# Optimization experiments

Hardware: AMD Instinct MI355X
Metric: run time of the kernel (lower is better)

Reference implementation:

```python
import jax, jax.numpy as jnp
import numpy as np

B, S, N = 128, 64, 32          # batch, self nodes, neighbors per node
INP_CAPS, OUT_CAPS, CAP_SZ = 8, 8, 16
K = OUT_CAPS
D = OUT_CAPS * CAP_SZ          # 128
C = D // K                     # capsule dim = 16
TAU = 1.0
EPS = 1e-12                    # F.normalize eps


def _l2norm(x):
    n = jnp.sqrt(jnp.sum(x * x, axis=-1, keepdims=True))
    return x / jnp.maximum(n, EPS)


def setup_inputs() -> dict:
    key = jax.random.key(0)
    k1, k2, k3, k4 = jax.random.split(key, 4)
    inp_d = INP_CAPS * CAP_SZ
    return {
        "self_vectors": jax.random.normal(k1, (B, S, inp_d), dtype=jnp.float32),
        "neighbor_vectors": jax.random.normal(k2, (B, S, N, inp_d), dtype=jnp.float32),
        "w1": jax.random.normal(k3, (inp_d, D), dtype=jnp.float32) * (1.0 / np.sqrt(inp_d)),
        "b1": jax.random.normal(k4, (D,), dtype=jnp.float32) * (1.0 / np.sqrt(D)),
        "max_iter": 3,
    }


def reference(self_vectors, neighbor_vectors, w1, b1, max_iter):
    inp_d = INP_CAPS * CAP_SZ
    self_z = jax.nn.relu(self_vectors.reshape(-1, inp_d) @ w1 + b1)
    neigh_z = jax.nn.relu(neighbor_vectors.reshape(-1, inp_d) @ w1 + b1)

    # [B,S,K,C] and [B,S,N,K,C], each capsule L2-normalized
    self_zn = _l2norm(self_z.reshape(B, S, K, C))
    neigh_zn = _l2norm(neigh_z.reshape(B, S, N, K, C))

    u = None
    for it in range(max_iter):
        if u is None:
            p = jnp.zeros((B, S, N, K), dtype=self_zn.dtype)
        else:
            # agreement scores: [B,S,N,K]
            p = jnp.einsum("bsnkc,bskc->bsnk", neigh_zn, u)
        p = jax.nn.softmax(p / TAU, axis=-1)
        # weighted neighbor sum over N -> [B,S,K,C]
        u = jnp.einsum("bsnkc,bsnk->bskc", neigh_zn, p) + self_zn
        if it < max_iter - 1:
            u = _l2norm(u)

    # dropout p=0.0 (eval) -> identity
    return jax.nn.relu(u.reshape(B, S, D))
```

## Files before the change

### kernel.cpp

```cpp
#include <hip/hip_runtime.h>
#include <hip/hip_bf16.h>


#define NB 32
#define DD 128
#define ZS 132
#define PPS 37


#define WSYNC() asm volatile("s_waitcnt lgkmcnt(0)" ::: "memory")

typedef __attribute__((ext_vector_type(8))) short bf16x8;
typedef __attribute__((ext_vector_type(4))) float f32x4;
typedef __attribute__((ext_vector_type(4))) float float4v;

__device__ __forceinline__ float bf16bits_to_f32(unsigned short u) {
  return __uint_as_float(((unsigned int)u) << 16);
}
__device__ __forceinline__ void split_bf16(float x, unsigned short& hi, unsigned short& lo) {
  unsigned int xb = __float_as_uint(x);
  hi = (unsigned short)(xb >> 16);
  float hif = __uint_as_float(xb & 0xFFFF0000u);
  float lof = x - hif;
  lo = (unsigned short)(__float_as_uint(lof) >> 16);
}
__device__ __forceinline__ void make_frag(float4v v0, float4v v1, bf16x8& h, bf16x8& l) {
#pragma unroll
  for (int i = 0; i < 4; ++i) {
    unsigned short hh, ll;
    split_bf16(v0[i], hh, ll);
    h[i] = (short)hh; l[i] = (short)ll;
    split_bf16(v1[i], hh, ll);
    h[4 + i] = (short)hh; l[4 + i] = (short)ll;
  }
}

__global__ void detect_kernel(const unsigned short* __restrict__ w1u,
                              int* __restrict__ flag) {
  int t = threadIdx.x;
  float v = bf16bits_to_f32(w1u[2 * t]);
  int hit = !(fabsf(v) < 1e4f);
  unsigned long long m = __ballot(hit);
  if (t == 0) flag[0] = (m != 0ull) ? 1 : 0;
}

__global__ __launch_bounds__(256) void swizzle_w_kernel(
    const void* __restrict__ w1, const int* __restrict__ flag,
    unsigned short* __restrict__ whi, unsigned short* __restrict__ wlo) {
  int idx = blockIdx.x * 256 + threadIdx.x;
  int k = idx >> 7, n = idx & 127;
  int kt = k >> 5, q = (k >> 3) & 3, j = k & 7;
  int nt = n >> 4, nl = n & 15;
  int lane = q * 16 + nl;
  int dst = ((kt * 8 + nt) * 64 + lane) * 8 + j;
  unsigned short hb, lb;
  if (*flag) {
    split_bf16(((const float*)w1)[idx], hb, lb);
  } else {
    hb = ((const unsigned short*)w1)[idx];
    lb = 0;
  }
  whi[dst] = hb;
  wlo[dst] = lb;
}

__global__ __launch_bounds__(64, 2) void routing_kernel(
    const void* __restrict__ selfv,
    const void* __restrict__ neighv,
    const unsigned short* __restrict__ whi,
    const unsigned short* __restrict__ wlo,
    const void* __restrict__ b1,
    void* __restrict__ out,
    const int* __restrict__ flag) {
  __shared__ __align__(16) float zn[33 * ZS];
  __shared__ __align__(16) float nrm[264];
  __shared__ __align__(16) float pp[8 * PPS];
  __shared__ __align__(16) float uu[128];

  const int lane = threadIdx.x;
  const int q = lane >> 4;
  const int ml = lane & 15;
  const size_t bs = blockIdx.x;
  const bool isf32 = (*flag != 0);

  const size_t noff = bs * (size_t)(NB * DD);
  const size_t soff = bs * (size_t)DD;

  f32x4 acc[3][8];
#pragma unroll
  for (int mt = 0; mt < 3; ++mt)
#pragma unroll
    for (int nt = 0; nt < 8; ++nt) acc[mt][nt] = (f32x4){0.f, 0.f, 0.f, 0.f};

#pragma unroll
  for (int kt = 0; kt < 4; ++kt) {
    const int col = kt * 32 + q * 8;
    bf16x8 a0h, a0l, a1h, a1l, a2h, a2l;
    if (isf32) {
      const float* nf = (const float*)neighv + noff;
      const float* sf = (const float*)selfv + soff;
      float4v v0 = *(const float4v*)(nf + (size_t)ml * DD + col);
      float4v v1 = *(const float4v*)(nf + (size_t)ml * DD + col + 4);
      make_frag(v0, v1, a0h, a0l);
      v0 = *(const float4v*)(nf + (size_t)(16 + ml) * DD + col);
      v1 = *(const float4v*)(nf + (size_t)(16 + ml) * DD + col + 4);
      make_frag(v0, v1, a1h, a1l);
      v0 = *(const float4v*)(sf + col);
      v1 = *(const float4v*)(sf + col + 4);
      make_frag(v0, v1, a2h, a2l);
    } else {
      const unsigned short* nbf = (const unsigned short*)neighv + noff;
      const unsigned short* sbf = (const unsigned short*)selfv + soff;
      const bf16x8 zv = (bf16x8){0, 0, 0, 0, 0, 0, 0, 0};
      a0h = *(const bf16x8*)(nbf + (size_t)ml * DD + col);
      a1h = *(const bf16x8*)(nbf + (size_t)(16 + ml) * DD + col);
      a2h = *(const bf16x8*)(sbf + col);
      a0l = zv; a1l = zv; a2l = zv;
    }
#pragma unroll
    for (int nt = 0; nt < 8; ++nt) {
      const size_t bo = ((size_t)(kt * 8 + nt) * 64 + lane) * 8;
      bf16x8 bh = *(const bf16x8*)(whi + bo);
      bf16x8 bl = *(const bf16x8*)(wlo + bo);
      acc[0][nt] = __builtin_amdgcn_mfma_f32_16x16x32_bf16(a0h, bh, acc[0][nt], 0, 0, 0);
      acc[1][nt] = __builtin_amdgcn_mfma_f32_16x16x32_bf16(a1h, bh, acc[1][nt], 0, 0, 0);
      acc[2][nt] = __builtin_amdgcn_mfma_f32_16x16x32_bf16(a2h, bh, acc[2][nt], 0, 0, 0);
      acc[0][nt] = __builtin_amdgcn_mfma_f32_16x16x32_bf16(a0h, bl, acc[0][nt], 0, 0, 0);
      acc[1][nt] = __builtin_amdgcn_mfma_f32_16x16x32_bf16(a1h, bl, acc[1][nt], 0, 0, 0);
      acc[2][nt] = __builtin_amdgcn_mfma_f32_16x16x32_bf16(a2h, bl, acc[2][nt], 0, 0, 0);
      acc[0][nt] = __builtin_amdgcn_mfma_f32_16x16x32_bf16(a0l, bh, acc[0][nt], 0, 0, 0);
      acc[1][nt] = __builtin_amdgcn_mfma_f32_16x16x32_bf16(a1l, bh, acc[1][nt], 0, 0, 0);
      acc[2][nt] = __builtin_amdgcn_mfma_f32_16x16x32_bf16(a2l, bh, acc[2][nt], 0, 0, 0);
    }
  }

  float bias[8];
#pragma unroll
  for (int nt = 0; nt < 8; ++nt) {
    const int c = nt * 16 + ml;
    bias[nt] = isf32 ? ((const float*)b1)[c]
                     : bf16bits_to_f32(((const unsigned short*)b1)[c]);
  }
#pragma unroll
  for (int mt = 0; mt < 2; ++mt)
#pragma unroll
    for (int nt = 0; nt < 8; ++nt)
#pragma unroll
      for (int r = 0; r < 4; ++r) {
        const int row = mt * 16 + q * 4 + r;
        zn[row * ZS + nt * 16 + ml] = fmaxf(acc[mt][nt][r] + bias[nt], 0.f);
      }
  if (q == 0) {
#pragma unroll
    for (int nt = 0; nt < 8; ++nt)
      zn[32 * ZS + nt * 16 + ml] = fmaxf(acc[2][nt][0] + bias[nt], 0.f);
  }
  WSYNC();

  for (int id = lane; id < 264; id += 64) {
    const int row = id >> 3, k = id & 7;
    const float4v* zp = (const float4v*)&zn[row * ZS + k * 16];
    float4v a = zp[0], b = zp[1], c = zp[2], d = zp[3];
    float ss = a[0]*a[0]+a[1]*a[1]+a[2]*a[2]+a[3]*a[3]
             + b[0]*b[0]+b[1]*b[1]+b[2]*b[2]+b[3]*b[3]
             + c[0]*c[0]+c[1]*c[1]+c[2]*c[2]+c[3]*c[3]
             + d[0]*d[0]+d[1]*d[1]+d[2]*d[2]+d[3]*d[3];
    nrm[id] = 1.f / fmaxf(sqrtf(ss), 1e-12f);
  }
  WSYNC();

  const int half = lane >> 5;
  const int k2 = (lane >> 2) & 7;
  const int c4 = lane & 3;
  const int k1 = lane & 7;
  const int ng = lane >> 3;

  for (int it = 0; it < 3; ++it) {
    if (it > 0) {
      const float4v* up = (const float4v*)&uu[k1 * 16];
      float4v U0 = up[0], U1 = up[1], U2 = up[2], U3 = up[3];
#pragma unroll
      for (int p = 0; p < 4; ++p) {
        const int n = ng + 8 * p;
        const float4v* zp = (const float4v*)&zn[n * ZS + k1 * 16];
        float4v z0 = zp[0], z1 = zp[1], z2 = zp[2], z3 = zp[3];
        float dot = U0[0]*z0[0]+U0[1]*z0[1]+U0[2]*z0[2]+U0[3]*z0[3]
                  + U1[0]*z1[0]+U1[1]*z1[1]+U1[2]*z1[2]+U1[3]*z1[3]
                  + U2[0]*z2[0]+U2[1]*z2[1]+U2[2]*z2[2]+U2[3]*z2[3]
                  + U3[0]*z3[0]+U3[1]*z3[1]+U3[2]*z3[2]+U3[3]*z3[3];
        const float nv = nrm[n * 8 + k1];
        const float lg = dot * nv;
        float m = lg;
        m = fmaxf(m, __shfl_xor(m, 1));
        m = fmaxf(m, __shfl_xor(m, 2));
        m = fmaxf(m, __shfl_xor(m, 4));
        float e = __expf(lg - m);
        float s = e;
        s += __shfl_xor(s, 1);
        s += __shfl_xor(s, 2);
        s += __shfl_xor(s, 4);
        pp[k1 * PPS + n] = (e / s) * nv;
      }
      WSYNC();
    }
    float4v a = (float4v){0.f, 0.f, 0.f, 0.f};
#pragma unroll
    for (int n0 = 0; n0 < 16; ++n0) {
      const int n = half * 16 + n0;
      const float w = (it == 0) ? nrm[n * 8 + k2] * 0.125f : pp[k2 * PPS + n];
      float4v z = *(const float4v*)&zn[n * ZS + k2 * 16 + c4 * 4];
      a[0] += w * z[0];
      a[1] += w * z[1];
      a[2] += w * z[2];
      a[3] += w * z[3];
    }
#pragma unroll
    for (int i = 0; i < 4; ++i) a[i] += __shfl_xor(a[i], 32);
    {
      float4v zs = *(const float4v*)&zn[32 * ZS + k2 * 16 + c4 * 4];
      const float sn = nrm[256 + k2];
      a[0] += sn * zs[0];
      a[1] += sn * zs[1];
      a[2] += sn * zs[2];
      a[3] += sn * zs[3];
    }
    if (it < 2) {
      float ss = a[0]*a[0] + a[1]*a[1] + a[2]*a[2] + a[3]*a[3];
      ss += __shfl_xor(ss, 1);
      ss += __shfl_xor(ss, 2);
      const float rn = 1.f / fmaxf(sqrtf(ss), 1e-12f);
      a[0] *= rn; a[1] *= rn; a[2] *= rn; a[3] *= rn;
      if (half == 0) *(float4v*)&uu[k2 * 16 + c4 * 4] = a;
      WSYNC();
    } else if (half == 0) {
      a[0] = (a[0] < 0.f) ? 0.f : a[0];
      a[1] = (a[1] < 0.f) ? 0.f : a[1];
      a[2] = (a[2] < 0.f) ? 0.f : a[2];
      a[3] = (a[3] < 0.f) ? 0.f : a[3];
      const size_t oidx = bs * DD + k2 * 16 + c4 * 4;
      if (isf32) {
        *(float4v*)((float*)out + oidx) = a;
      } else {
        unsigned int w0, w1;
        unsigned int x0 = __float_as_uint(a[0]);
        unsigned int x1 = __float_as_uint(a[1]);
        unsigned int x2 = __float_as_uint(a[2]);
        unsigned int x3 = __float_as_uint(a[3]);
        x0 += 0x7fffu + ((x0 >> 16) & 1u);
        x1 += 0x7fffu + ((x1 >> 16) & 1u);
        x2 += 0x7fffu + ((x2 >> 16) & 1u);
        x3 += 0x7fffu + ((x3 >> 16) & 1u);
        w0 = (x0 >> 16) | (x1 & 0xFFFF0000u);
        w1 = (x2 >> 16) | (x3 & 0xFFFF0000u);
        ((unsigned int*)out)[oidx / 2] = w0;
        ((unsigned int*)out)[oidx / 2 + 1] = w1;
      }
    }
  }
}

extern "C" void kernel_launch(void* const* d_in, const int* in_sizes, int n_in,
                              void* d_out, int out_size, void* d_ws, size_t ws_size,
                              hipStream_t stream) {
  (void)in_sizes; (void)n_in; (void)out_size; (void)ws_size;
  const void* selfv = d_in[0];
  const void* neighv = d_in[1];
  const void* w1 = d_in[2];
  const void* b1 = d_in[3];
  int* flag = (int*)d_ws;
  unsigned short* whi = (unsigned short*)((char*)d_ws + 64);
  unsigned short* wlo = (unsigned short*)((char*)d_ws + 64 + 32768);

  detect_kernel<<<1, 64, 0, stream>>>((const unsigned short*)w1, flag);
  swizzle_w_kernel<<<64, 256, 0, stream>>>(w1, flag, whi, wlo);
  routing_kernel<<<8192, 64, 0, stream>>>(selfv, neighv, whi, wlo, b1, d_out, flag);
}
```

Baseline: 242.5 us.

## Split self-capsule GEMM into separate kernel and keep routing in MFMA registers

Self-vector projection and normalization move into a new batched kernel that writes normalized self capsules to the output buffer. The routing kernel then computes only the 32 neighbor rows and runs all routing iterations directly on the MFMA accumulator registers, using DPP 16-lane reductions instead of LDS staging. This removes shared memory and the wasted third MFMA tile, so more blocks can be resident per CU. In exchange it adds an extra kernel launch plus a global round-trip for the self capsules, and the softmax weights are rounded to bf16 with the max-subtraction dropped.

```diff
diff --git a/kernel.cpp b/kernel.cpp
--- a/kernel.cpp
+++ b/kernel.cpp
@@ -2,13 +2,7 @@
 #include <hip/hip_bf16.h>
 
 
-#define NB 32
 #define DD 128
-#define ZS 132
-#define PPS 37
-
-
-#define WSYNC() asm volatile("s_waitcnt lgkmcnt(0)" ::: "memory")
 
 typedef __attribute__((ext_vector_type(8))) short bf16x8;
 typedef __attribute__((ext_vector_type(4))) float f32x4;
@@ -33,6 +27,29 @@
     split_bf16(v1[i], hh, ll);
     h[4 + i] = (short)hh; l[4 + i] = (short)ll;
   }
+}
+
+template <int CTRL>
+__device__ __forceinline__ float dpp_add(float x) {
+  int y = __builtin_amdgcn_update_dpp(0, __float_as_int(x), CTRL, 0xf, 0xf, true);
+  return x + __int_as_float(y);
+}
+__device__ __forceinline__ float sum16(float x) {
+  x = dpp_add<0xB1>(x);
+  x = dpp_add<0x4E>(x);
+  x = dpp_add<0x124>(x);
+  x = dpp_add<0x128>(x);
+  return x;
+}
+
+__device__ __forceinline__ unsigned pack_bf16(float a, float b) {
+  return (__float_as_uint(a) >> 16) | (__float_as_uint(b) & 0xFFFF0000u);
+}
+__device__ __forceinline__ float unpack_lo(unsigned w) {
+  return __uint_as_float(w << 16);
+}
+__device__ __forceinline__ float unpack_hi(unsigned w) {
+  return __uint_as_float(w & 0xFFFF0000u);
 }
 
 __global__ void detect_kernel(const unsigned short* __restrict__ w1u,
@@ -64,58 +81,115 @@
   wlo[dst] = lb;
 }
 
-__global__ __launch_bounds__(64, 2) void routing_kernel(
+__global__ __launch_bounds__(64, 4) void selfz_kernel(
     const void* __restrict__ selfv,
+    const unsigned short* __restrict__ whi,
+    const unsigned short* __restrict__ wlo,
+    const void* __restrict__ b1,
+    void* __restrict__ out,
+    const int* __restrict__ flag) {
+  const int lane = threadIdx.x;
+  const int q = lane >> 4, ml = lane & 15;
+  const int base = blockIdx.x * 16;
+  const bool isf32 = (*flag != 0);
+
+  f32x4 acc[8];
+#pragma unroll
+  for (int nt = 0; nt < 8; ++nt) acc[nt] = (f32x4){0.f, 0.f, 0.f, 0.f};
+
+#pragma unroll
+  for (int kt = 0; kt < 4; ++kt) {
+    const int col = kt * 32 + q * 8;
+    bf16x8 ah, al;
+    if (isf32) {
+      const float* sf = (const float*)selfv + (size_t)(base + ml) * DD + col;
+      make_frag(*(const float4v*)sf, *(const float4v*)(sf + 4), ah, al);
+    } else {
+      ah = *(const bf16x8*)((const unsigned short*)selfv + (size_t)(base + ml) * DD + col);
+      al = (bf16x8){0, 0, 0, 0, 0, 0, 0, 0};
+    }
+#pragma unroll
+    for (int nt = 0; nt < 8; ++nt) {
+      const size_t bo = ((size_t)(kt * 8 + nt) * 64 + lane) * 8;
+      bf16x8 bh = *(const bf16x8*)(whi + bo);
+      bf16x8 bl = *(const bf16x8*)(wlo + bo);
+      acc[nt] = __builtin_amdgcn_mfma_f32_16x16x32_bf16(ah, bh, acc[nt], 0, 0, 0);
+      acc[nt] = __builtin_amdgcn_mfma_f32_16x16x32_bf16(ah, bl, acc[nt], 0, 0, 0);
+      acc[nt] = __builtin_amdgcn_mfma_f32_16x16x32_bf16(al, bh, acc[nt], 0, 0, 0);
+    }
+  }
+#pragma unroll
+  for (int nt = 0; nt < 8; ++nt) {
+    const float bv = isf32 ? ((const float*)b1)[nt * 16 + ml]
+                           : bf16bits_to_f32(((const unsigned short*)b1)[nt * 16 + ml]);
+#pragma unroll
+    for (int r = 0; r < 4; ++r) acc[nt][r] = fmaxf(acc[nt][r] + bv, 0.f);
+  }
+#pragma unroll
+  for (int r = 0; r < 4; ++r)
+#pragma unroll
+    for (int nt = 0; nt < 8; ++nt) {
+      float ss = sum16(acc[nt][r] * acc[nt][r]);
+      acc[nt][r] *= 1.f / fmaxf(sqrtf(ss), 1e-12f);
+    }
+#pragma unroll
+  for (int r = 0; r < 4; ++r)
+#pragma unroll
+    for (int nt = 0; nt < 8; ++nt) {
+      const size_t o = (size_t)(base + q * 4 + r) * DD + nt * 16 + ml;
+      if (isf32) {
+        ((float*)out)[o] = acc[nt][r];
+      } else {
+        unsigned int xb = __float_as_uint(acc[nt][r]);
+        ((unsigned short*)out)[o] =
+            (unsigned short)((xb + 0x7fffu + ((xb >> 16) & 1u)) >> 16);
+      }
+    }
+}
+
+__global__ __launch_bounds__(64, 4) void routing_kernel(
     const void* __restrict__ neighv,
     const unsigned short* __restrict__ whi,
     const unsigned short* __restrict__ wlo,
     const void* __restrict__ b1,
     void* __restrict__ out,
     const int* __restrict__ flag) {
-  __shared__ __align__(16) float zn[33 * ZS];
-  __shared__ __align__(16) float nrm[264];
-  __shared__ __align__(16) float pp[8 * PPS];
-  __shared__ __align__(16) float uu[128];
-
   const int lane = threadIdx.x;
-  const int q = lane >> 4;
-  const int ml = lane & 15;
+  const int q = lane >> 4, ml = lane & 15;
   const size_t bs = blockIdx.x;
   const bool isf32 = (*flag != 0);
 
-  const size_t noff = bs * (size_t)(NB * DD);
-  const size_t soff = bs * (size_t)DD;
-
-  f32x4 acc[3][8];
-#pragma unroll
-  for (int mt = 0; mt < 3; ++mt)
+  float zs[8];
+#pragma unroll
+  for (int nt = 0; nt < 8; ++nt) {
+    const size_t o = bs * DD + nt * 16 + ml;
+    zs[nt] = isf32 ? ((const float*)out)[o]
+                   : bf16bits_to_f32(((const unsigned short*)out)[o]);
+  }
+
+  f32x4 acc[2][8];
+#pragma unroll
+  for (int mt = 0; mt < 2; ++mt)
 #pragma unroll
     for (int nt = 0; nt < 8; ++nt) acc[mt][nt] = (f32x4){0.f, 0.f, 0.f, 0.f};
 
+  const size_t noff = bs * (size_t)(32 * DD);
 #pragma unroll
   for (int kt = 0; kt < 4; ++kt) {
     const int col = kt * 32 + q * 8;
-    bf16x8 a0h, a0l, a1h, a1l, a2h, a2l;
+    bf16x8 a0h, a0l, a1h, a1l;
     if (isf32) {
       const float* nf = (const float*)neighv + noff;
-      const float* sf = (const float*)selfv + soff;
-      float4v v0 = *(const float4v*)(nf + (size_t)ml * DD + col);
-      float4v v1 = *(const float4v*)(nf + (size_t)ml * DD + col + 4);
-      make_frag(v0, v1, a0h, a0l);
-      v0 = *(const float4v*)(nf + (size_t)(16 + ml) * DD + col);
-      v1 = *(const float4v*)(nf + (size_t)(16 + ml) * DD + col + 4);
-      make_frag(v0, v1, a1h, a1l);
-      v0 = *(const float4v*)(sf + col);
-      v1 = *(const float4v*)(sf + col + 4);
-      make_frag(v0, v1, a2h, a2l);
+      const float* p0 = nf + (size_t)ml * DD + col;
+      const float* p1 = nf + (size_t)(16 + ml) * DD + col;
+      make_frag(*(const float4v*)p0, *(const float4v*)(p0 + 4), a0h, a0l);
+      make_frag(*(const float4v*)p1, *(const float4v*)(p1 + 4), a1h, a1l);
     } else {
       const unsigned short* nbf = (const unsigned short*)neighv + noff;
-      const unsigned short* sbf = (const unsigned short*)selfv + soff;
-      const bf16x8 zv = (bf16x8){0, 0, 0, 0, 0, 0, 0, 0};
       a0h = *(const bf16x8*)(nbf + (size_t)ml * DD + col);
       a1h = *(const bf16x8*)(nbf + (size_t)(16 + ml) * DD + col);
-      a2h = *(const bf16x8*)(sbf + col);
-      a0l = zv; a1l = zv; a2l = zv;
+      a0l = (bf16x8){0, 0, 0, 0, 0, 0, 0, 0};
+      a1l = a0l;
     }
 #pragma unroll
     for (int nt = 0; nt < 8; ++nt) {
@@ -124,136 +198,102 @@
       bf16x8 bl = *(const bf16x8*)(wlo + bo);
       acc[0][nt] = __builtin_amdgcn_mfma_f32_16x16x32_bf16(a0h, bh, acc[0][nt], 0, 0, 0);
       acc[1][nt] = __builtin_amdgcn_mfma_f32_16x16x32_bf16(a1h, bh, acc[1][nt], 0, 0, 0);
-      acc[2][nt] = __builtin_amdgcn_mfma_f32_16x16x32_bf16(a2h, bh, acc[2][nt], 0, 0, 0);
       acc[0][nt] = __builtin_amdgcn_mfma_f32_16x16x32_bf16(a0h, bl, acc[0][nt], 0, 0, 0);
       acc[1][nt] = __builtin_amdgcn_mfma_f32_16x16x32_bf16(a1h, bl, acc[1][nt], 0, 0, 0);
-      acc[2][nt] = __builtin_amdgcn_mfma_f32_16x16x32_bf16(a2h, bl, acc[2][nt], 0, 0, 0);
       acc[0][nt] = __builtin_amdgcn_mfma_f32_16x16x32_bf16(a0l, bh, acc[0][nt], 0, 0, 0);
       acc[1][nt] = __builtin_amdgcn_mfma_f32_16x16x32_bf16(a1l, bh, acc[1][nt], 0, 0, 0);
-      acc[2][nt] = __builtin_amdgcn_mfma_f32_16x16x32_bf16(a2l, bh, acc[2][nt], 0, 0, 0);
-    }
-  }
-
-  float bias[8];
-#pragma unroll
-  for (int nt = 0; nt < 8; ++nt) {
-    const int c = nt * 16 + ml;
-    bias[nt] = isf32 ? ((const float*)b1)[c]
-                     : bf16bits_to_f32(((const unsigned short*)b1)[c]);
+    }
+  }
+
+#pragma unroll
+  for (int nt = 0; nt < 8; ++nt) {
+    const float bv = isf32 ? ((const float*)b1)[nt * 16 + ml]
+                           : bf16bits_to_f32(((const unsigned short*)b1)[nt * 16 + ml]);
+#pragma unroll
+    for (int mt = 0; mt < 2; ++mt)
+#pragma unroll
+      for (int r = 0; r < 4; ++r) acc[mt][nt][r] = fmaxf(acc[mt][nt][r] + bv, 0.f);
   }
 #pragma unroll
   for (int mt = 0; mt < 2; ++mt)
 #pragma unroll
-    for (int nt = 0; nt < 8; ++nt)
+    for (int r = 0; r < 4; ++r)
+#pragma unroll
+      for (int nt = 0; nt < 8; ++nt) {
+        float ss = sum16(acc[mt][nt][r] * acc[mt][nt][r]);
+        acc[mt][nt][r] *= 1.f / fmaxf(sqrtf(ss), 1e-12f);
+      }
+
+  float u[8];
+#pragma unroll
+  for (int nt = 0; nt < 8; ++nt) {
+    float t = acc[0][nt][0] + acc[0][nt][1] + acc[0][nt][2] + acc[0][nt][3] +
+              acc[1][nt][0] + acc[1][nt][1] + acc[1][nt][2] + acc[1][nt][3];
+    t += __shfl_xor(t, 16);
+    t += __shfl_xor(t, 32);
+    u[nt] = t * 0.125f + zs[nt];
+  }
+#pragma unroll
+  for (int nt = 0; nt < 8; ++nt) {
+    float ss = sum16(u[nt] * u[nt]);
+    u[nt] *= 1.f / fmaxf(sqrtf(ss), 1e-12f);
+  }
+
+  unsigned wp[2][4][4];
+#pragma unroll
+  for (int it = 1; it < 3; ++it) {
+#pragma unroll
+    for (int mt = 0; mt < 2; ++mt)
 #pragma unroll
       for (int r = 0; r < 4; ++r) {
-        const int row = mt * 16 + q * 4 + r;
-        zn[row * ZS + nt * 16 + ml] = fmaxf(acc[mt][nt][r] + bias[nt], 0.f);
-      }
+        float e[8];
+        float s = 0.f;
+#pragma unroll
+        for (int nt = 0; nt < 8; ++nt) {
+          float l = sum16(acc[mt][nt][r] * u[nt]);
+          e[nt] = __expf(l);
+          s += e[nt];
+        }
+        const float inv = 1.f / s;
+#pragma unroll
+        for (int j = 0; j < 4; ++j)
+          wp[mt][r][j] = pack_bf16(e[2 * j] * inv, e[2 * j + 1] * inv);
+      }
+#pragma unroll
+    for (int nt = 0; nt < 8; ++nt) {
+      float t = 0.f;
+#pragma unroll
+      for (int mt = 0; mt < 2; ++mt)
+#pragma unroll
+        for (int r = 0; r < 4; ++r) {
+          const unsigned w = wp[mt][r][nt >> 1];
+          const float p = (nt & 1) ? unpack_hi(w) : unpack_lo(w);
+          t = fmaf(p, acc[mt][nt][r], t);
+        }
+      t += __shfl_xor(t, 16);
+      t += __shfl_xor(t, 32);
+      u[nt] = t + zs[nt];
+    }
+    if (it < 2) {
+#pragma unroll
+      for (int nt = 0; nt < 8; ++nt) {
+        float ss = sum16(u[nt] * u[nt]);
+        u[nt] *= 1.f / fmaxf(sqrtf(ss), 1e-12f);
+      }
+    }
+  }
+
   if (q == 0) {
 #pragma unroll
-    for (int nt = 0; nt < 8; ++nt)
-      zn[32 * ZS + nt * 16 + ml] = fmaxf(acc[2][nt][0] + bias[nt], 0.f);
-  }
-  WSYNC();
-
-  for (int id = lane; id < 264; id += 64) {
-    const int row = id >> 3, k = id & 7;
-    const float4v* zp = (const float4v*)&zn[row * ZS + k * 16];
-    float4v a = zp[0], b = zp[1], c = zp[2], d = zp[3];
-    float ss = a[0]*a[0]+a[1]*a[1]+a[2]*a[2]+a[3]*a[3]
-             + b[0]*b[0]+b[1]*b[1]+b[2]*b[2]+b[3]*b[3]
-             + c[0]*c[0]+c[1]*c[1]+c[2]*c[2]+c[3]*c[3]
-             + d[0]*d[0]+d[1]*d[1]+d[2]*d[2]+d[3]*d[3];
-    nrm[id] = 1.f / fmaxf(sqrtf(ss), 1e-12f);
-  }
-  WSYNC();
-
-  const int half = lane >> 5;
-  const int k2 = (lane >> 2) & 7;
-  const int c4 = lane & 3;
-  const int k1 = lane & 7;
-  const int ng = lane >> 3;
-
-  for (int it = 0; it < 3; ++it) {
-    if (it > 0) {
-      const float4v* up = (const float4v*)&uu[k1 * 16];
-      float4v U0 = up[0], U1 = up[1], U2 = up[2], U3 = up[3];
-#pragma unroll
-      for (int p = 0; p < 4; ++p) {
-        const int n = ng + 8 * p;
-        const float4v* zp = (const float4v*)&zn[n * ZS + k1 * 16];
-        float4v z0 = zp[0], z1 = zp[1], z2 = zp[2], z3 = zp[3];
-        float dot = U0[0]*z0[0]+U0[1]*z0[1]+U0[2]*z0[2]+U0[3]*z0[3]
-                  + U1[0]*z1[0]+U1[1]*z1[1]+U1[2]*z1[2]+U1[3]*z1[3]
-                  + U2[0]*z2[0]+U2[1]*z2[1]+U2[2]*z2[2]+U2[3]*z2[3]
-                  + U3[0]*z3[0]+U3[1]*z3[1]+U3[2]*z3[2]+U3[3]*z3[3];
-        const float nv = nrm[n * 8 + k1];
-        const float lg = dot * nv;
-        float m = lg;
-        m = fmaxf(m, __shfl_xor(m, 1));
-        m = fmaxf(m, __shfl_xor(m, 2));
-        m = fmaxf(m, __shfl_xor(m, 4));
-        float e = __expf(lg - m);
-        float s = e;
-        s += __shfl_xor(s, 1);
-        s += __shfl_xor(s, 2);
-        s += __shfl_xor(s, 4);
-        pp[k1 * PPS + n] = (e / s) * nv;
-      }
-      WSYNC();
-    }
-    float4v a = (float4v){0.f, 0.f, 0.f, 0.f};
-#pragma unroll
-    for (int n0 = 0; n0 < 16; ++n0) {
-      const int n = half * 16 + n0;
-      const float w = (it == 0) ? nrm[n * 8 + k2] * 0.125f : pp[k2 * PPS + n];
-      float4v z = *(const float4v*)&zn[n * ZS + k2 * 16 + c4 * 4];
-      a[0] += w * z[0];
-      a[1] += w * z[1];
-      a[2] += w * z[2];
-      a[3] += w * z[3];
-    }
-#pragma unroll
-    for (int i = 0; i < 4; ++i) a[i] += __shfl_xor(a[i], 32);
-    {
-      float4v zs = *(const float4v*)&zn[32 * ZS + k2 * 16 + c4 * 4];
-      const float sn = nrm[256 + k2];
-      a[0] += sn * zs[0];
-      a[1] += sn * zs[1];
-      a[2] += sn * zs[2];
-      a[3] += sn * zs[3];
-    }
-    if (it < 2) {
-      float ss = a[0]*a[0] + a[1]*a[1] + a[2]*a[2] + a[3]*a[3];
-      ss += __shfl_xor(ss, 1);
-      ss += __shfl_xor(ss, 2);
-      const float rn = 1.f / fmaxf(sqrtf(ss), 1e-12f);
-      a[0] *= rn; a[1] *= rn; a[2] *= rn; a[3] *= rn;
-      if (half == 0) *(float4v*)&uu[k2 * 16 + c4 * 4] = a;
-      WSYNC();
-    } else if (half == 0) {
-      a[0] = (a[0] < 0.f) ? 0.f : a[0];
-      a[1] = (a[1] < 0.f) ? 0.f : a[1];
-      a[2] = (a[2] < 0.f) ? 0.f : a[2];
-      a[3] = (a[3] < 0.f) ? 0.f : a[3];
-      const size_t oidx = bs * DD + k2 * 16 + c4 * 4;
+    for (int nt = 0; nt < 8; ++nt) {
+      float r = (u[nt] < 0.f) ? 0.f : u[nt];
+      const size_t o = bs * DD + nt * 16 + ml;
       if (isf32) {
-        *(float4v*)((float*)out + oidx) = a;
+        ((float*)out)[o] = r;
       } else {
-        unsigned int w0, w1;
-        unsigned int x0 = __float_as_uint(a[0]);
-        unsigned int x1 = __float_as_uint(a[1]);
-        unsigned int x2 = __float_as_uint(a[2]);
-        unsigned int x3 = __float_as_uint(a[3]);
-        x0 += 0x7fffu + ((x0 >> 16) & 1u);
-        x1 += 0x7fffu + ((x1 >> 16) & 1u);
-        x2 += 0x7fffu + ((x2 >> 16) & 1u);
-        x3 += 0x7fffu + ((x3 >> 16) & 1u);
-        w0 = (x0 >> 16) | (x1 & 0xFFFF0000u);
-        w1 = (x2 >> 16) | (x3 & 0xFFFF0000u);
-        ((unsigned int*)out)[oidx / 2] = w0;
-        ((unsigned int*)out)[oidx / 2 + 1] = w1;
+        unsigned int xb = __float_as_uint(r);
+        ((unsigned short*)out)[o] =
+            (unsigned short)((xb + 0x7fffu + ((xb >> 16) & 1u)) >> 16);
       }
     }
   }
@@ -273,5 +313,6 @@
 
   detect_kernel<<<1, 64, 0, stream>>>((const unsigned short*)w1, flag);
   swizzle_w_kernel<<<64, 256, 0, stream>>>(w1, flag, whi, wlo);
-  routing_kernel<<<8192, 64, 0, stream>>>(selfv, neighv, whi, wlo, b1, d_out, flag);
-}
+  selfz_kernel<<<512, 64, 0, stream>>>(selfv, whi, wlo, b1, d_out, flag);
+  routing_kernel<<<8192, 64, 0, stream>>>(neighv, whi, wlo, b1, d_out, flag);
+}
```

Measured after the change: 308.5 us. +27.2%, slower.
